# Kernel tuning notes

Hardware: AMD Instinct MI355X
Metric: run time of the kernel (lower is better)

Reference implementation:

```python
import jax, jax.numpy as jnp
import numpy as np

B, N, C = 4, 4096, 256
NUM_HEADS = 8
NUM_GROUPS = 4  # num_groups2, recursive_index=True path
HEAD_DIM = C // NUM_HEADS
SCALE = HEAD_DIM ** -0.5


def setup_inputs() -> dict:
    key = jax.random.key(0)
    k_x, k_idx, k_qkv, k_proj, k_pb = jax.random.split(key, 5)
    x = jax.random.normal(k_x, (B, N, C), dtype=jnp.float32)
    idx = jax.random.permutation(k_idx, N)  # random token shuffle (torch.randperm)
    # nn.Linear params (torch convention: y = x @ W.T + b)
    w_qkv = jax.random.normal(k_qkv, (3 * C, C), dtype=jnp.float32) * (1.0 / np.sqrt(C))
    w_proj = jax.random.normal(k_proj, (C, C), dtype=jnp.float32) * (1.0 / np.sqrt(C))
    b_proj = jax.random.normal(k_pb, (C,), dtype=jnp.float32) * 0.01
    return {"x": x, "idx": idx, "w_qkv": w_qkv, "w_proj": w_proj, "b_proj": b_proj}


def reference(x, idx, w_qkv, w_proj, b_proj):
    g, H, d = NUM_GROUPS, NUM_HEADS, HEAD_DIM
    n = N // g  # tokens per group
    inverse = jnp.argsort(idx)
    xp = x[:, idx, :]  # shuffled tokens [B, N, C]
    # qkv projection then split into groups/heads: [B, g, n, 3, H, d]
    qkv = (xp @ w_qkv.T).reshape(B, g, n, 3, H, d)
    q = qkv[:, :, :, 0].transpose(0, 1, 3, 2, 4)  # [B, g, H, n, d]
    k = qkv[:, :, :, 1].transpose(0, 1, 3, 2, 4)
    v = qkv[:, :, :, 2].transpose(0, 1, 3, 2, 4)
    attn = jnp.einsum('bghnd,bghmd->bghnm', q, k) * SCALE  # [B, g, H, n, n]
    attn = jax.nn.softmax(attn, axis=-1)
    o = jnp.einsum('bghnm,bghmd->bghnd', attn, v)
    # [B, g, H, n, d] -> [B, g, n, H, d] -> [B, N, C] (group-major token order)
    o = o.transpose(0, 1, 3, 2, 4).reshape(B, N, C)
    o = o[:, inverse, :]  # undo the shuffle
    return o @ w_proj.T + b_proj
```

## Files before the change

### kernel.cpp

```cpp
#include <hip/hip_runtime.h>
#include <hip/hip_bf16.h>


typedef __attribute__((ext_vector_type(8))) short bf16x8;
typedef __attribute__((ext_vector_type(4))) float f32x4;

__device__ __forceinline__ unsigned short f2bf(float x){
  __hip_bfloat16 h = __float2bfloat16(x);
  return __builtin_bit_cast(unsigned short, h);
}

__device__ __forceinline__ bf16x8 cvt8(const float4 f0, const float4 f1){
  bf16x8 v;
  v[0]=(short)f2bf(f0.x); v[1]=(short)f2bf(f0.y);
  v[2]=(short)f2bf(f0.z); v[3]=(short)f2bf(f0.w);
  v[4]=(short)f2bf(f1.x); v[5]=(short)f2bf(f1.y);
  v[6]=(short)f2bf(f1.z); v[7]=(short)f2bf(f1.w);
  return v;
}

#define QSCALE (0.17677669529663687f * 1.4426950408889634f)


__global__ __launch_bounds__(256, 3) void qkv_gemm(
    const float* __restrict__ x, const int* __restrict__ idx,
    const float* __restrict__ w_qkv,
    unsigned short* __restrict__ Qb, unsigned short* __restrict__ KF,
    unsigned short* __restrict__ VF)
{
  __shared__ __align__(16) unsigned short Asl[128*64];
  __shared__ __align__(16) unsigned short Bsl[128*64];
  const int tid = threadIdx.x;
  const int bx = blockIdx.x, by = blockIdx.y;
  const int m0 = bx << 7;
  const int bb = bx >> 5;
  const int gg = (bx >> 3) & 3;
  const int j0 = (bx & 31) << 7;
  const int n0 = by << 7;

  int srow[2], brow[2], wb[2];
  #pragma unroll
  for (int it = 0; it < 2; ++it){
    int c = (it << 8) + tid;
    int row = c >> 2;
    int k8 = (c & 3) << 3;
    srow[it] = (bb << 12) + idx[j0 + row];
    brow[it] = n0 + row;
    wb[it] = ((row << 7) + (k8 << 1)) ^ ((row & 7) << 4);
  }

  #pragma unroll
  for (int it = 0; it < 2; ++it){
    int k8 = (((it << 8) + tid) & 3) << 3;
    const float* xs = x + srow[it]*256 + k8;
    const float* wsp = w_qkv + brow[it]*256 + k8;
    *(bf16x8*)((char*)Asl + wb[it]) = cvt8(*(const float4*)(xs), *(const float4*)(xs+4));
    *(bf16x8*)((char*)Bsl + wb[it]) = cvt8(*(const float4*)(wsp), *(const float4*)(wsp+4));
  }
  __syncthreads();

  const int lane = tid & 63;
  const int w = tid >> 6, wr = w >> 1, wc = w & 1;
  const int lr = lane & 15, lg = lane >> 4;
  const int ka = lg << 3;

  f32x4 acc[4][4];
  #pragma unroll
  for (int il = 0; il < 4; ++il)
    #pragma unroll
    for (int jl = 0; jl < 4; ++jl)
      acc[il][jl] = (f32x4){0.f,0.f,0.f,0.f};

  for (int st = 0; st < 8; ++st){
    float4 a0[2], a1[2], c0[2], c1[2];
    const bool pf = (st < 7);
    if (pf){
      int kb = (st + 1) << 5;
      #pragma unroll
      for (int it = 0; it < 2; ++it){
        int k8 = (((it << 8) + tid) & 3) << 3;
        const float* xs = x + srow[it]*256 + kb + k8;
        const float* wsp = w_qkv + brow[it]*256 + kb + k8;
        a0[it] = *(const float4*)(xs);  a1[it] = *(const float4*)(xs + 4);
        c0[it] = *(const float4*)(wsp); c1[it] = *(const float4*)(wsp + 4);
      }
    }

    bf16x8 af[4], bfr[4];
    #pragma unroll
    for (int il = 0; il < 4; ++il){
      int rowA = (wr << 6) + (il << 4) + lr;
      af[il] = *(const bf16x8*)((const char*)Asl + (((rowA << 7) + (ka << 1)) ^ ((rowA & 7) << 4)));
      int rowB = (wc << 6) + (il << 4) + lr;
      bfr[il] = *(const bf16x8*)((const char*)Bsl + (((rowB << 7) + (ka << 1)) ^ ((rowB & 7) << 4)));
    }
    __builtin_amdgcn_s_setprio(1);
    #pragma unroll
    for (int il = 0; il < 4; ++il)
      #pragma unroll
      for (int jl = 0; jl < 4; ++jl)
        acc[il][jl] = __builtin_amdgcn_mfma_f32_16x16x32_bf16(af[il], bfr[jl], acc[il][jl], 0, 0, 0);
    __builtin_amdgcn_s_setprio(0);

    __syncthreads();
    if (pf){
      #pragma unroll
      for (int it = 0; it < 2; ++it){
        *(bf16x8*)((char*)Asl + wb[it]) = cvt8(a0[it], a1[it]);
        *(bf16x8*)((char*)Bsl + wb[it]) = cvt8(c0[it], c1[it]);
      }
      __syncthreads();
    }
  }

  const int s = by >> 1;
  const int hbase = ((bb << 2) + gg) << 3;
  #pragma unroll
  for (int il = 0; il < 4; ++il){
    int mr0 = m0 + (wr << 6) + (il << 4) + (lg << 2);
    int nl0 = mr0 & 1023;
    int t   = nl0 >> 5;
    #pragma unroll
    for (int jl = 0; jl < 4; ++jl){
      int ocol = ((by & 1) << 7) + (wc << 6) + (jl << 4) + lr;
      int h  = ocol >> 5, dd = ocol & 31;
      int head = hbase + h;
      if (s == 2){
        int m = nl0 & 31;
        int lane2 = ((m >> 3) << 4) + (dd & 15);
        int half = dd >> 4;
        ushort4 pk;
        pk.x = f2bf(acc[il][jl][0]); pk.y = f2bf(acc[il][jl][1]);
        pk.z = f2bf(acc[il][jl][2]); pk.w = f2bf(acc[il][jl][3]);
        *(ushort4*)(VF + head*32768 + t*1024 + half*512 + lane2*8 + (m & 7)) = pk;
      } else if (s == 1){
        int r0 = nl0 & 31;
        int f  = (r0 >> 2) & 1;
        unsigned short* dst = KF + head*32768 + t*1024 + f*512
                             + ((((dd >> 3) << 4) + ((r0 >> 3) << 2)) << 3) + (dd & 7);
        dst[0]  = f2bf(acc[il][jl][0]);
        dst[8]  = f2bf(acc[il][jl][1]);
        dst[16] = f2bf(acc[il][jl][2]);
        dst[24] = f2bf(acc[il][jl][3]);
      } else {
        unsigned short* dst = Qb + head*32768 + dd;
        #pragma unroll
        for (int q = 0; q < 4; ++q)
          dst[(nl0 + q) << 5] = f2bf(acc[il][jl][q] * QSCALE);
      }
    }
  }
}

__device__ __forceinline__ void softmax16(
    const f32x4 s0, const f32x4 s1, const f32x4 s2, const f32x4 s3,
    bf16x8& pf0, bf16x8& pf1)
{
  float p0=__builtin_amdgcn_exp2f(s0[0]);  float p1=__builtin_amdgcn_exp2f(s0[1]);
  float p2=__builtin_amdgcn_exp2f(s0[2]);  float p3=__builtin_amdgcn_exp2f(s0[3]);
  float p4=__builtin_amdgcn_exp2f(s1[0]);  float p5=__builtin_amdgcn_exp2f(s1[1]);
  float p6=__builtin_amdgcn_exp2f(s1[2]);  float p7=__builtin_amdgcn_exp2f(s1[3]);
  float p8=__builtin_amdgcn_exp2f(s2[0]);  float p9=__builtin_amdgcn_exp2f(s2[1]);
  float p10=__builtin_amdgcn_exp2f(s2[2]); float p11=__builtin_amdgcn_exp2f(s2[3]);
  float p12=__builtin_amdgcn_exp2f(s3[0]); float p13=__builtin_amdgcn_exp2f(s3[1]);
  float p14=__builtin_amdgcn_exp2f(s3[2]); float p15=__builtin_amdgcn_exp2f(s3[3]);

  pf0[0]=(short)f2bf(p0);  pf0[1]=(short)f2bf(p1);
  pf0[2]=(short)f2bf(p2);  pf0[3]=(short)f2bf(p3);
  pf0[4]=(short)f2bf(p4);  pf0[5]=(short)f2bf(p5);
  pf0[6]=(short)f2bf(p6);  pf0[7]=(short)f2bf(p7);
  pf1[0]=(short)f2bf(p8);  pf1[1]=(short)f2bf(p9);
  pf1[2]=(short)f2bf(p10); pf1[3]=(short)f2bf(p11);
  pf1[4]=(short)f2bf(p12); pf1[5]=(short)f2bf(p13);
  pf1[6]=(short)f2bf(p14); pf1[7]=(short)f2bf(p15);
}

__global__ __launch_bounds__(256, 2) void attn_kernel(
    const unsigned short* __restrict__ Qb, const unsigned short* __restrict__ KF,
    const unsigned short* __restrict__ VF, unsigned short* __restrict__ OB)
{
  __shared__ __align__(16) char lds[32768];
  const int tid  = threadIdx.x;
  const int bid  = blockIdx.x;
  const int b    = ((bid & 7) << 6) + (bid >> 3);
  const int head = b >> 2;
  const int qblk = b & 3;
  const int lane = tid & 63;
  const int w  = tid >> 6;
  const int lr = lane & 15, lg = lane >> 4;
  const int q0 = qblk * 256 + w * 64;

  const unsigned short* kf = KF + head*32768;
  const unsigned short* vf = VF + head*32768;
  const unsigned short* qbase = Qb + head*32768;

  {
    bf16x8 k0 = *(const bf16x8*)(kf + tid*8);
    bf16x8 k1 = *(const bf16x8*)(kf + 2048 + tid*8);
    bf16x8 v0 = *(const bf16x8*)(vf + tid*8);
    bf16x8 v1 = *(const bf16x8*)(vf + 2048 + tid*8);
    *(bf16x8*)(lds + tid*16)          = k0;
    *(bf16x8*)(lds + 4096 + tid*16)   = k1;
    *(bf16x8*)(lds + 8192 + tid*16)   = v0;
    *(bf16x8*)(lds + 12288 + tid*16)  = v1;
  }

  bf16x8 qf[4];
  #pragma unroll
  for (int g = 0; g < 4; ++g)
    qf[g] = *(const bf16x8*)(qbase + (q0 + g*16 + lr)*32 + (lg << 3));

  const short one_bf = (short)0x3F80;
  bf16x8 onesf = {one_bf,one_bf,one_bf,one_bf,one_bf,one_bf,one_bf,one_bf};

  f32x4 o0[4], o1[4], ls[4];
  #pragma unroll
  for (int g = 0; g < 4; ++g){
    o0[g] = (f32x4){0.f,0.f,0.f,0.f};
    o1[g] = (f32x4){0.f,0.f,0.f,0.f};
    ls[g] = (f32x4){0.f,0.f,0.f,0.f};
  }
  const f32x4 zz={0.f,0.f,0.f,0.f};

  __syncthreads();
  int cur = 0;
  for (int it = 0; it < 8; ++it){
    bf16x8 kr0, kr1, vr0, vr1;
    const bool pfch = (it < 7);
    if (pfch){
      const unsigned short* kg = kf + (it+1)*4096 + tid*8;
      const unsigned short* vg = vf + (it+1)*4096 + tid*8;
      kr0 = *(const bf16x8*)(kg);
      kr1 = *(const bf16x8*)(kg + 2048);
      vr0 = *(const bf16x8*)(vg);
      vr1 = *(const bf16x8*)(vg + 2048);
    }

    const char* KL = lds + cur*16384 + lane*16;
    const char* VL = KL + 8192;
    #pragma unroll
    for (int hh = 0; hh < 2; ++hh){
      const char* kp_ = KL + hh*4096;
      const char* vp_ = VL + hh*4096;
      bf16x8 kA0 = *(const bf16x8*)(kp_);
      bf16x8 kB0 = *(const bf16x8*)(kp_ + 1024);
      bf16x8 kA1 = *(const bf16x8*)(kp_ + 2048);
      bf16x8 kB1 = *(const bf16x8*)(kp_ + 3072);
      bf16x8 v00 = *(const bf16x8*)(vp_);
      bf16x8 v01 = *(const bf16x8*)(vp_ + 1024);
      bf16x8 v10 = *(const bf16x8*)(vp_ + 2048);
      bf16x8 v11 = *(const bf16x8*)(vp_ + 3072);

      __builtin_amdgcn_s_setprio(1);
      f32x4 sA0 = __builtin_amdgcn_mfma_f32_16x16x32_bf16(kA0, qf[0], zz, 0, 0, 0);
      f32x4 sB0 = __builtin_amdgcn_mfma_f32_16x16x32_bf16(kB0, qf[0], zz, 0, 0, 0);
      f32x4 sA1 = __builtin_amdgcn_mfma_f32_16x16x32_bf16(kA1, qf[0], zz, 0, 0, 0);
      f32x4 sB1 = __builtin_amdgcn_mfma_f32_16x16x32_bf16(kB1, qf[0], zz, 0, 0, 0);
      __builtin_amdgcn_s_setprio(0);

      #pragma unroll
      for (int g = 0; g < 4; ++g){
        f32x4 nA0, nB0, nA1, nB1;
        if (g < 3){
          __builtin_amdgcn_s_setprio(1);
          nA0 = __builtin_amdgcn_mfma_f32_16x16x32_bf16(kA0, qf[g+1], zz, 0, 0, 0);
          nB0 = __builtin_amdgcn_mfma_f32_16x16x32_bf16(kB0, qf[g+1], zz, 0, 0, 0);
          nA1 = __builtin_amdgcn_mfma_f32_16x16x32_bf16(kA1, qf[g+1], zz, 0, 0, 0);
          nB1 = __builtin_amdgcn_mfma_f32_16x16x32_bf16(kB1, qf[g+1], zz, 0, 0, 0);
          __builtin_amdgcn_s_setprio(0);
        }
        bf16x8 pf0, pf1;
        softmax16(sA0, sB0, sA1, sB1, pf0, pf1);
        __builtin_amdgcn_s_setprio(1);
        o0[g] = __builtin_amdgcn_mfma_f32_16x16x32_bf16(pf0, v00, o0[g], 0, 0, 0);
        o1[g] = __builtin_amdgcn_mfma_f32_16x16x32_bf16(pf0, v01, o1[g], 0, 0, 0);
        o0[g] = __builtin_amdgcn_mfma_f32_16x16x32_bf16(pf1, v10, o0[g], 0, 0, 0);
        o1[g] = __builtin_amdgcn_mfma_f32_16x16x32_bf16(pf1, v11, o1[g], 0, 0, 0);
        ls[g] = __builtin_amdgcn_mfma_f32_16x16x32_bf16(pf0, onesf, ls[g], 0, 0, 0);
        ls[g] = __builtin_amdgcn_mfma_f32_16x16x32_bf16(pf1, onesf, ls[g], 0, 0, 0);
        __builtin_amdgcn_s_setprio(0);
        if (g < 3){ sA0 = nA0; sB0 = nB0; sA1 = nA1; sB1 = nB1; }
      }
    }

    if (pfch){
      char* db = lds + (cur^1)*16384;
      *(bf16x8*)(db + tid*16)          = kr0;
      *(bf16x8*)(db + 4096 + tid*16)   = kr1;
      *(bf16x8*)(db + 8192 + tid*16)   = vr0;
      *(bf16x8*)(db + 12288 + tid*16)  = vr1;
    }
    __syncthreads();
    cur ^= 1;
  }

  const int bI = head >> 5, gI = (head >> 3) & 3, hI = head & 7;
  unsigned short* obase = OB + (bI*4096 + gI*1024 + q0)*256 + hI*32;
  #pragma unroll
  for (int g = 0; g < 4; ++g){
    #pragma unroll
    for (int q = 0; q < 4; ++q){
      float iv = 1.0f / ls[g][q];
      int r = (g << 4) + (lg << 2) + q;
      obase[r*256 + lr]      = f2bf(o0[g][q] * iv);
      obase[r*256 + 16 + lr] = f2bf(o1[g][q] * iv);
    }
  }
}

__global__ __launch_bounds__(256) void proj_gemm(
    const unsigned short* __restrict__ OB, const float* __restrict__ w_proj,
    const float* __restrict__ b_proj, const int* __restrict__ idx,
    float* __restrict__ out)
{
  __shared__ unsigned short Alds[64*256];
  __shared__ unsigned short Blds[64*256];
  const int tid = threadIdx.x;
  const int m0 = blockIdx.x << 6;
  const int bb = m0 >> 12;

  #pragma unroll
  for (int it = 0; it < 8; ++it){
    int c = (it << 8) + tid;
    int row = c >> 5;
    int k8 = (c & 31) << 3;
    int byt = ((row << 9) + (k8 << 1)) ^ ((row & 7) << 4);
    *(bf16x8*)((char*)Alds + byt) = *(const bf16x8*)(OB + (m0+row)*256 + k8);
  }

  const int w  = tid >> 6, lane = tid & 63;
  const int lr = lane & 15, lg = lane >> 4;
  const int wr = w >> 1,  wc = w & 1;

  for (int nt = 0; nt < 2; ++nt){
    const int n0 = blockIdx.y * 128 + nt * 64;
    __syncthreads();
    #pragma unroll
    for (int it = 0; it < 8; ++it){
      int c = (it << 8) + tid;
      int row = c >> 5;
      int k8 = (c & 31) << 3;
      const float4 f0 = *(const float4*)(w_proj + (n0+row)*256 + k8);
      const float4 f1 = *(const float4*)(w_proj + (n0+row)*256 + k8 + 4);
      bf16x8 v;
      v[0]=(short)f2bf(f0.x); v[1]=(short)f2bf(f0.y);
      v[2]=(short)f2bf(f0.z); v[3]=(short)f2bf(f0.w);
      v[4]=(short)f2bf(f1.x); v[5]=(short)f2bf(f1.y);
      v[6]=(short)f2bf(f1.z); v[7]=(short)f2bf(f1.w);
      int byt = ((row << 9) + (k8 << 1)) ^ ((row & 7) << 4);
      *(bf16x8*)((char*)Blds + byt) = v;
    }
    __syncthreads();

    f32x4 acc[2][2];
    #pragma unroll
    for (int i=0;i<2;++i)
      #pragma unroll
      for (int j=0;j<2;++j)
        acc[i][j] = (f32x4){0.f,0.f,0.f,0.f};

    #pragma unroll
    for (int ks = 0; ks < 8; ++ks){
      bf16x8 af[2], bfr[2];
      int ka = (ks << 5) + (lg << 3);
      #pragma unroll
      for (int i=0;i<2;++i){
        int rowA = (wr << 5) + (i << 4) + lr;
        int bytA = ((rowA << 9) + (ka << 1)) ^ ((rowA & 7) << 4);
        af[i] = *(const bf16x8*)((const char*)Alds + bytA);
        int rowB = (wc << 5) + (i << 4) + lr;
        int bytB = ((rowB << 9) + (ka << 1)) ^ ((rowB & 7) << 4);
        bfr[i] = *(const bf16x8*)((const char*)Blds + bytB);
      }
      #pragma unroll
      for (int i=0;i<2;++i)
        #pragma unroll
        for (int j=0;j<2;++j)
          acc[i][j] = __builtin_amdgcn_mfma_f32_16x16x32_bf16(af[i], bfr[j], acc[i][j], 0, 0, 0);
    }

    #pragma unroll
    for (int i=0;i<2;++i){
      int mr0 = m0 + (wr << 5) + (i << 4) + (lg << 2);
      int rd[4];
      #pragma unroll
      for (int q=0;q<4;++q)
        rd[q] = (bb << 12) + idx[(mr0 + q) & 4095];
      #pragma unroll
      for (int j=0;j<2;++j){
        int o = n0 + (wc << 5) + (j << 4) + lr;
        float bias = b_proj[o];
        #pragma unroll
        for (int q=0;q<4;++q)
          out[rd[q]*256 + o] = acc[i][j][q] + bias;
      }
    }
  }
}

extern "C" void kernel_launch(void* const* d_in, const int* in_sizes, int n_in,
                              void* d_out, int out_size, void* d_ws, size_t ws_size,
                              hipStream_t stream)
{
  const float* x      = (const float*)d_in[0];
  const int*   idx    = (const int*)  d_in[1];
  const float* w_qkv  = (const float*)d_in[2];
  const float* w_proj = (const float*)d_in[3];
  const float* b_proj = (const float*)d_in[4];
  float* out = (float*)d_out;

  char* ws = (char*)d_ws;
  unsigned short* Qb = (unsigned short*)(ws);
  unsigned short* KF = (unsigned short*)(ws + (8u  << 20));
  unsigned short* VF = (unsigned short*)(ws + (16u << 20));
  unsigned short* OB = (unsigned short*)(ws + (24u << 20));

  qkv_gemm<<<dim3(128, 6), 256, 0, stream>>>(x, idx, w_qkv, Qb, KF, VF);
  attn_kernel<<<dim3(512), 256, 0, stream>>>(Qb, KF, VF, OB);
  proj_gemm<<<dim3(256, 2), 256, 0, stream>>>(OB, w_proj, b_proj, idx, out);
}
```

Measured before the change: 56.14 us.

## Pipeline proj GEMM over K with register prefetch and smaller LDS tiles

The projection GEMM now walks K in 32-wide slices instead of loading the full 256-wide A and B tiles up front. The next slice is prefetched into registers while MFMAs run on the current slice. LDS use drops from 64KB to about 24KB, so launch_bounds(256,2) lets more blocks share a CU. Each block now covers a 64x128 output tile in one pass with wider per-wave accumulators instead of two 64-column passes, at the cost of more __syncthreads per block.

```diff
diff --git a/kernel.cpp b/kernel.cpp
--- a/kernel.cpp
+++ b/kernel.cpp
@@ -308,92 +308,107 @@
   }
 }
 
-__global__ __launch_bounds__(256) void proj_gemm(
+__global__ __launch_bounds__(256, 2) void proj_gemm(
     const unsigned short* __restrict__ OB, const float* __restrict__ w_proj,
     const float* __restrict__ b_proj, const int* __restrict__ idx,
     float* __restrict__ out)
 {
-  __shared__ unsigned short Alds[64*256];
-  __shared__ unsigned short Blds[64*256];
+  __shared__ __align__(16) unsigned short Asl[64*64];
+  __shared__ __align__(16) unsigned short Bsl[128*64];
   const int tid = threadIdx.x;
-  const int m0 = blockIdx.x << 6;
-  const int bb = m0 >> 12;
-
-  #pragma unroll
-  for (int it = 0; it < 8; ++it){
+  const int bx = blockIdx.x, by = blockIdx.y;
+  const int m0 = bx << 6;
+  const int bb = bx >> 6;
+  const int n0 = by << 7;
+
+  const int rowAs = tid >> 2, k8A = (tid & 3) << 3;
+  const int wbA = ((rowAs << 7) + (k8A << 1)) ^ ((rowAs & 7) << 4);
+  int browB[2], wbB[2], k8B[2];
+  #pragma unroll
+  for (int it = 0; it < 2; ++it){
     int c = (it << 8) + tid;
-    int row = c >> 5;
-    int k8 = (c & 31) << 3;
-    int byt = ((row << 9) + (k8 << 1)) ^ ((row & 7) << 4);
-    *(bf16x8*)((char*)Alds + byt) = *(const bf16x8*)(OB + (m0+row)*256 + k8);
-  }
-
-  const int w  = tid >> 6, lane = tid & 63;
+    int row = c >> 2;
+    k8B[it] = (c & 3) << 3;
+    browB[it] = n0 + row;
+    wbB[it] = ((row << 7) + (k8B[it] << 1)) ^ ((row & 7) << 4);
+  }
+
+  *(bf16x8*)((char*)Asl + wbA) = *(const bf16x8*)(OB + (m0 + rowAs)*256 + k8A);
+  #pragma unroll
+  for (int it = 0; it < 2; ++it){
+    const float* wsp = w_proj + browB[it]*256 + k8B[it];
+    *(bf16x8*)((char*)Bsl + wbB[it]) = cvt8(*(const float4*)(wsp), *(const float4*)(wsp+4));
+  }
+  __syncthreads();
+
+  const int lane = tid & 63;
+  const int w = tid >> 6, wr = w & 1, wc = w >> 1;
   const int lr = lane & 15, lg = lane >> 4;
-  const int wr = w >> 1,  wc = w & 1;
-
-  for (int nt = 0; nt < 2; ++nt){
-    const int n0 = blockIdx.y * 128 + nt * 64;
+  const int ka = lg << 3;
+
+  f32x4 acc[2][4];
+  #pragma unroll
+  for (int il = 0; il < 2; ++il)
+    #pragma unroll
+    for (int jl = 0; jl < 4; ++jl)
+      acc[il][jl] = (f32x4){0.f,0.f,0.f,0.f};
+
+  for (int st = 0; st < 8; ++st){
+    bf16x8 aN; float4 b0[2], b1[2];
+    const bool pf = (st < 7);
+    if (pf){
+      int kb = (st + 1) << 5;
+      aN = *(const bf16x8*)(OB + (m0 + rowAs)*256 + kb + k8A);
+      #pragma unroll
+      for (int it = 0; it < 2; ++it){
+        const float* wsp = w_proj + browB[it]*256 + kb + k8B[it];
+        b0[it] = *(const float4*)(wsp); b1[it] = *(const float4*)(wsp + 4);
+      }
+    }
+
+    bf16x8 af[2], bfr[4];
+    #pragma unroll
+    for (int il = 0; il < 2; ++il){
+      int rowA = (wr << 5) + (il << 4) + lr;
+      af[il] = *(const bf16x8*)((const char*)Asl + (((rowA << 7) + (ka << 1)) ^ ((rowA & 7) << 4)));
+    }
+    #pragma unroll
+    for (int jl = 0; jl < 4; ++jl){
+      int rowB = (wc << 6) + (jl << 4) + lr;
+      bfr[jl] = *(const bf16x8*)((const char*)Bsl + (((rowB << 7) + (ka << 1)) ^ ((rowB & 7) << 4)));
+    }
+    __builtin_amdgcn_s_setprio(1);
+    #pragma unroll
+    for (int il = 0; il < 2; ++il)
+      #pragma unroll
+      for (int jl = 0; jl < 4; ++jl)
+        acc[il][jl] = __builtin_amdgcn_mfma_f32_16x16x32_bf16(af[il], bfr[jl], acc[il][jl], 0, 0, 0);
+    __builtin_amdgcn_s_setprio(0);
+
     __syncthreads();
-    #pragma unroll
-    for (int it = 0; it < 8; ++it){
-      int c = (it << 8) + tid;
-      int row = c >> 5;
-      int k8 = (c & 31) << 3;
-      const float4 f0 = *(const float4*)(w_proj + (n0+row)*256 + k8);
-      const float4 f1 = *(const float4*)(w_proj + (n0+row)*256 + k8 + 4);
-      bf16x8 v;
-      v[0]=(short)f2bf(f0.x); v[1]=(short)f2bf(f0.y);
-      v[2]=(short)f2bf(f0.z); v[3]=(short)f2bf(f0.w);
-      v[4]=(short)f2bf(f1.x); v[5]=(short)f2bf(f1.y);
-      v[6]=(short)f2bf(f1.z); v[7]=(short)f2bf(f1.w);
-      int byt = ((row << 9) + (k8 << 1)) ^ ((row & 7) << 4);
-      *(bf16x8*)((char*)Blds + byt) = v;
-    }
-    __syncthreads();
-
-    f32x4 acc[2][2];
-    #pragma unroll
-    for (int i=0;i<2;++i)
-      #pragma unroll
-      for (int j=0;j<2;++j)
-        acc[i][j] = (f32x4){0.f,0.f,0.f,0.f};
-
-    #pragma unroll
-    for (int ks = 0; ks < 8; ++ks){
-      bf16x8 af[2], bfr[2];
-      int ka = (ks << 5) + (lg << 3);
-      #pragma unroll
-      for (int i=0;i<2;++i){
-        int rowA = (wr << 5) + (i << 4) + lr;
-        int bytA = ((rowA << 9) + (ka << 1)) ^ ((rowA & 7) << 4);
-        af[i] = *(const bf16x8*)((const char*)Alds + bytA);
-        int rowB = (wc << 5) + (i << 4) + lr;
-        int bytB = ((rowB << 9) + (ka << 1)) ^ ((rowB & 7) << 4);
-        bfr[i] = *(const bf16x8*)((const char*)Blds + bytB);
-      }
-      #pragma unroll
-      for (int i=0;i<2;++i)
-        #pragma unroll
-        for (int j=0;j<2;++j)
-          acc[i][j] = __builtin_amdgcn_mfma_f32_16x16x32_bf16(af[i], bfr[j], acc[i][j], 0, 0, 0);
-    }
-
-    #pragma unroll
-    for (int i=0;i<2;++i){
-      int mr0 = m0 + (wr << 5) + (i << 4) + (lg << 2);
-      int rd[4];
-      #pragma unroll
-      for (int q=0;q<4;++q)
-        rd[q] = (bb << 12) + idx[(mr0 + q) & 4095];
-      #pragma unroll
-      for (int j=0;j<2;++j){
-        int o = n0 + (wc << 5) + (j << 4) + lr;
-        float bias = b_proj[o];
-        #pragma unroll
-        for (int q=0;q<4;++q)
-          out[rd[q]*256 + o] = acc[i][j][q] + bias;
-      }
+    if (pf){
+      *(bf16x8*)((char*)Asl + wbA) = aN;
+      #pragma unroll
+      for (int it = 0; it < 2; ++it)
+        *(bf16x8*)((char*)Bsl + wbB[it]) = cvt8(b0[it], b1[it]);
+      __syncthreads();
+    }
+  }
+
+  #pragma unroll
+  for (int il = 0; il < 2; ++il){
+    int mr0 = m0 + (wr << 5) + (il << 4) + (lg << 2);
+    int rd[4];
+    #pragma unroll
+    for (int q = 0; q < 4; ++q)
+      rd[q] = (bb << 12) + idx[(mr0 + q) & 4095];
+    #pragma unroll
+    for (int jl = 0; jl < 4; ++jl){
+      int o = n0 + (wc << 6) + (jl << 4) + lr;
+      float bias = b_proj[o];
+      #pragma unroll
+      for (int q = 0; q < 4; ++q)
+        out[rd[q]*256 + o] = acc[il][jl][q] + bias;
     }
   }
 }
```

Result: slower. 58.88 us (+4.9%).
